# Kernel optimization log

Hardware: AMD Instinct MI355X
Metric: run time of the kernel (lower is better)

Reference implementation:

```python
import jax, jax.numpy as jnp
import numpy as np

# ---- static config (matches init_kwargs) ----
B, H, W = 4, 256, 256
TIN, F, P = 10, 4, 8          # time steps in, forecast steps, patch size
CIN = TIN + 2                  # x concatenated with 2-channel grid
E = 768                        # LATENT_DIMS
NB, BS = 8, 96                 # num_blocks, block_size = E // NB
HP, WP = H // P, W // P
MID = 4 * E                    # channel-mixer hidden (MLP_RATIO=4)
DEPTH = 4
LAM = 0.01                     # softshrink sparsity_threshold


def _gelu(t):
    return jax.nn.gelu(t, approximate=False)  # torch default GELU (erf)


def _shrink(t):
    return jnp.sign(t) * jnp.maximum(jnp.abs(t) - LAM, 0.0)


def _spectral(x, w1, b1, w2, b2):
    """SpectralConvBlockDiag: rfft2 -> block-diag complex MLP (GELU) -> softshrink -> irfft2 + residual."""
    bias = x
    b_, h_, w_, c_ = x.shape
    wf = w_ // 2 + 1
    xf = jnp.fft.rfft2(x, axes=(1, 2), norm='ortho').reshape(b_, h_, wf, NB, BS)
    xr, xi = jnp.real(xf), jnp.imag(xf)
    mm = lambda t, w: jnp.einsum('bhfni,nio->bhfno', t, w)
    # complex linear 1 + GELU on real/imag separately
    o1r = _gelu(mm(xr, w1[0]) - mm(xi, w1[1]) + b1[0])
    o1i = _gelu(mm(xi, w1[0]) + mm(xr, w1[1]) + b1[1])
    # complex linear 2 + softshrink
    o2r = _shrink(mm(o1r, w2[0]) - mm(o1i, w2[1]) + b2[0])
    o2i = _shrink(mm(o1i, w2[0]) + mm(o1r, w2[1]) + b2[1])
    xf = (o2r + 1j * o2i).reshape(b_, h_, wf, c_)
    out = jnp.fft.irfft2(xf, s=(h_, w_), axes=(1, 2), norm='ortho')
    return out + bias


def setup_inputs() -> dict:
    key = jax.random.key(0)
    ks = jax.random.split(key, 20)
    s = 0.02
    f32 = jnp.float32
    return {
        'x': jax.random.normal(ks[0], (B, H, W, TIN), f32),
        'grid': jax.random.uniform(ks[1], (B, H, W, 2), f32),
        'conv_w': s * jax.random.normal(ks[2], (E, CIN, P, P), f32),
        'conv_b': s * jax.random.normal(ks[3], (E,), f32),
        'pos_emb': s * jax.random.normal(ks[4], (HP, WP, E), f32),
        'w1': s * jax.random.normal(ks[5], (DEPTH, 2, NB, BS, BS), f32),
        'b1': s * jax.random.normal(ks[6], (DEPTH, 2, NB, BS), f32),
        'w2': s * jax.random.normal(ks[7], (DEPTH, 2, NB, BS, BS), f32),
        'b2': s * jax.random.normal(ks[8], (DEPTH, 2, NB, BS), f32),
        'fc1_w': s * jax.random.normal(ks[9], (DEPTH, E, MID), f32),
        'fc1_b': s * jax.random.normal(ks[10], (DEPTH, MID), f32),
        'fc2_w': s * jax.random.normal(ks[11], (DEPTH, MID, E), f32),
        'fc2_b': s * jax.random.normal(ks[12], (DEPTH, E), f32),
        'head_w1': s * jax.random.normal(ks[13], (E, 2 * E), f32),
        'head_b1': s * jax.random.normal(ks[14], (2 * E,), f32),
        'head_w2': s * jax.random.normal(ks[15], (2 * E, P * P), f32),
        'head_b2': s * jax.random.normal(ks[16], (P * P,), f32),
    }


def reference(x, grid, conv_w, conv_b, pos_emb, w1, b1, w2, b2,
              fc1_w, fc1_b, fc2_w, fc2_b, head_w1, head_b1, head_w2, head_b2):
    # concat grid channels and patch-embed (conv stride==kernel == patch einsum)
    z = jnp.concatenate([x, grid], axis=-1)                  # (B,H,W,CIN)
    patches = z.reshape(B, HP, P, WP, P, CIN)
    t = jnp.einsum('bhpwqc,ecpq->bhwe', patches, conv_w) + conv_b + pos_emb  # (B,HP,WP,E)
    states = []
    for _ in range(F):
        for d in range(DEPTH):                               # AFNOBoundariesBlock (no residual, identity norms)
            t = _spectral(t, w1[d], b1[d], w2[d], b2[d])
            t = _gelu(t @ fc1_w[d] + fc1_b[d]) @ fc2_w[d] + fc2_b[d]
        states.append(t)
    ls = jnp.stack(states, axis=1)                           # (B,F,HP,WP,E)
    h = _gelu(ls @ head_w1 + head_b1) @ head_w2 + head_b2    # (B,F,HP,WP,P*P)
    h = h.reshape(B, F, HP, WP, P, P, 1)
    h = jnp.transpose(h, (0, 6, 2, 4, 3, 5, 1)).reshape(B, 1, H, W, F)
    return jnp.squeeze(h, axis=1)                            # (B,H,W,F)
```

## Files before the change

### kernel.cpp

```cpp
#include <hip/hip_runtime.h>
#include <hip/hip_bf16.h>
#include <math.h>


typedef __attribute__((ext_vector_type(8))) _Float16 half8;
typedef __attribute__((ext_vector_type(4))) _Float16 half4v;
typedef __attribute__((ext_vector_type(4))) float float4v;

__device__ __forceinline__ float gelu_f(float v) {
    return 0.5f * v * (1.0f + erff(v * 0.70710678118654752f));
}
__device__ __forceinline__ float shrink_f(float v) {
    return (v > 0.01f) ? (v - 0.01f) : ((v < -0.01f) ? (v + 0.01f) : 0.0f);
}

#define STEP32 0.19634954084936207f

__device__ __forceinline__ void async16(const void* g, void* l) {
    __builtin_amdgcn_global_load_lds(
        (const __attribute__((address_space(1))) unsigned int*)g,
        (__attribute__((address_space(3))) unsigned int*)l, 16, 0, 0);
}

__global__ __launch_bounds__(256) void gather_patch(const float* __restrict__ x,
        const float* __restrict__ grd, _Float16* __restrict__ A)
{
    int idx = blockIdx.x * 256 + threadIdx.x;
    int j   = idx % 768;
    int tok = idx / 768;
    int c = j >> 6, p = (j >> 3) & 7, q = j & 7;
    int wp = tok & 31, hp = (tok >> 5) & 31, b = tok >> 10;
    int hh = hp * 8 + p, ww = wp * 8 + q;
    float v;
    if (c < 10) v = x[((b * 256 + hh) * 256 + ww) * 10 + c];
    else        v = grd[((b * 256 + hh) * 256 + ww) * 2 + (c - 10)];
    A[idx] = (_Float16)v;
}

__global__ __launch_bounds__(256) void dft_fwd_w(const _Float16* __restrict__ th,
        _Float16* __restrict__ Xr, _Float16* __restrict__ Xi)
{
    __shared__ float2 lut[32];
    int bh = blockIdx.x;
    int tid = threadIdx.x;
    if (tid < 32) { float a = tid * STEP32; lut[tid] = make_float2(cosf(a), sinf(a)); }
    __syncthreads();
    int b = bh >> 5, h = bh & 31;
    int c = blockIdx.y * 256 + tid;
    float v[32];
    #pragma unroll
    for (int w = 0; w < 32; ++w) v[w] = (float)th[(bh * 32 + w) * 768 + c];
    for (int kw = 0; kw <= 16; ++kw) {
        float ar = 0.f, ai = 0.f;
        #pragma unroll
        for (int w = 0; w < 32; ++w) {
            float2 cs = lut[(kw * w) & 31];
            ar += v[w] * cs.x;
            ai -= v[w] * cs.y;
        }
        size_t g = ((size_t)(b * 17 + kw) * 32 + h) * 768 + c;
        Xr[g] = (_Float16)(ar * 0.03125f);
        Xi[g] = (_Float16)(ai * 0.03125f);
    }
}

__global__ __launch_bounds__(256) void idft_w_mfma(const _Float16* __restrict__ Yr,
        const _Float16* __restrict__ Yi, _Float16* __restrict__ th)
{
    __shared__ alignas(16) _Float16 Yt[192 * 40];
    __shared__ alignas(16) _Float16 El[32 * 40];

    const int tid  = threadIdx.x;
    const int wave = tid >> 6;
    const int lane = tid & 63;
    const int lr   = lane & 15;
    const int quad = lane >> 4;

    const int bh = blockIdx.x;
    const int b  = bh >> 5, h = bh & 31;
    const int c0 = blockIdx.y * 192;

    for (int i = tid; i < 1024; i += 256) {
        int w = i >> 5, s = i & 31;
        float val;
        if (s <= 16) {
            float g = (s == 0 || s == 16) ? 1.f : 2.f;
            val = g * cosf(((w * s) & 31) * STEP32) * 0.03125f;
        } else {
            int k = s - 16;
            val = -2.f * sinf(((w * k) & 31) * STEP32) * 0.03125f;
        }
        El[w * 40 + s] = (_Float16)val;
    }

    #pragma unroll
    for (int i = 0; i < 3; ++i) {
        int u    = tid + i * 256;
        int slot = u / 24;
        int cg   = u % 24;
        const _Float16* src;
        if (slot < 17) src = Yr + ((size_t)(b * 17 + slot) * 32 + h) * 768;
        else           src = Yi + ((size_t)(b * 17 + (slot - 16)) * 32 + h) * 768;
        half8 v = *(const half8*)(src + c0 + cg * 8);
        #pragma unroll
        for (int e = 0; e < 8; ++e) {
            int el = e ^ (cg & 7);
            Yt[(cg * 8 + el) * 40 + slot] = v[el];
        }
    }
    __syncthreads();

    half8 af[2], bf[3];
    #pragma unroll
    for (int m = 0; m < 2; ++m)
        af[m] = *(const half8*)&El[(m * 16 + lr) * 40 + quad * 8];
    #pragma unroll
    for (int n = 0; n < 3; ++n)
        bf[n] = *(const half8*)&Yt[(wave * 48 + n * 16 + lr) * 40 + quad * 8];
    float4v acc[2][3];
    #pragma unroll
    for (int m = 0; m < 2; ++m)
        #pragma unroll
        for (int n = 0; n < 3; ++n) {
            float4v z = {0.f, 0.f, 0.f, 0.f};
            acc[m][n] = __builtin_amdgcn_mfma_f32_16x16x32_f16(af[m], bf[n], z, 0, 0, 0);
        }

    #pragma unroll
    for (int m = 0; m < 2; ++m)
        #pragma unroll
        for (int n = 0; n < 3; ++n) {
            int c = c0 + wave * 48 + n * 16 + lr;
            #pragma unroll
            for (int r = 0; r < 4; ++r) {
                int w = m * 16 + quad * 4 + r;
                size_t gi = (size_t)(bh * 32 + w) * 768 + c;
                th[gi] = (_Float16)(acc[m][n][r] + (float)th[gi]);
            }
        }
}

__global__ __launch_bounds__(256) void prep_specw(const float* __restrict__ w1,
        const float* __restrict__ w2, _Float16* __restrict__ out)
{
    __shared__ float tile[96][97];
    int mid = blockIdx.x;
    int n  = mid & 7;
    int ri = (mid >> 3) & 1;
    int l  = (mid >> 4) & 1;
    int d  = mid >> 5;
    const float* src = (l ? w2 : w1) + ((size_t)(d * 2 + ri) * 8 + n) * 9216;
    for (int idx = threadIdx.x; idx < 9216; idx += 256)
        tile[idx / 96][idx % 96] = src[idx];
    __syncthreads();
    _Float16* dst = out + (size_t)mid * 9216;
    for (int idx = threadIdx.x; idx < 9216; idx += 256)
        dst[idx] = (_Float16)tile[idx % 96][idx / 96];
}

__global__ __launch_bounds__(768) void spec_fused(
        _Float16* __restrict__ Xr, _Float16* __restrict__ Xi,
        const _Float16* __restrict__ W1r, const _Float16* __restrict__ W1i,
        const _Float16* __restrict__ W2r, const _Float16* __restrict__ W2i,
        const float* __restrict__ b1r, const float* __restrict__ b1i,
        const float* __restrict__ b2r, const float* __restrict__ b2i)
{
    __shared__ alignas(16) _Float16 Ec[1024], Es[1024];
    __shared__ alignas(16) _Float16 XTr[3840], XTi[3840];
    __shared__ alignas(16) _Float16 Zr[3328], Zi[3328];
    __shared__ alignas(16) _Float16 Sr[3328], Si[3328];

    const int bk = blockIdx.x;
    const int n  = blockIdx.y;
    const int tid = threadIdx.x;
    const int wave = tid >> 6, lane = tid & 63;
    const int wr = wave / 6;
    const int wo = wave % 6;
    const int lr = lane & 15, quad = lane >> 4;
    const size_t base = (size_t)bk * 24576 + n * 96;

    for (int i = tid; i < 1024; i += 768) {
        int kh = i >> 5, h = i & 31;
        float a = ((kh * h) & 31) * STEP32;
        Ec[i] = (_Float16)cosf(a);
        Es[i] = (_Float16)sinf(a);
    }
    for (int i = tid; i < 384; i += 768) {
        int h = i / 12, cc = (i % 12) * 8;
        half8 vr = *(const half8*)(Xr + base + (size_t)h * 768 + cc);
        half8 vi = *(const half8*)(Xi + base + (size_t)h * 768 + cc);
        #pragma unroll
        for (int e = 0; e < 8; ++e) {
            XTr[(cc + e) * 40 + h] = vr[e];
            XTi[(cc + e) * 40 + h] = vi[e];
        }
    }
    __syncthreads();

    const _Float16* w1r = W1r + (size_t)n * 9216;
    const _Float16* w1i = W1i + (size_t)n * 9216;
    const _Float16* w2r = W2r + (size_t)n * 9216;
    const _Float16* w2i = W2i + (size_t)n * 9216;

    half8 eC = *(const half8*)&Ec[(wr * 16 + lr) * 32 + quad * 8];
    half8 eS = *(const half8*)&Es[(wr * 16 + lr) * 32 + quad * 8];
    half8 eSn = -eS;

    {
        int c = wo * 16 + lr;
        float4v zr = {0,0,0,0}, zi = {0,0,0,0};
        half8 xr = *(const half8*)&XTr[c * 40 + quad * 8];
        half8 xi = *(const half8*)&XTi[c * 40 + quad * 8];
        zr = __builtin_amdgcn_mfma_f32_16x16x32_f16(eC,  xr, zr, 0, 0, 0);
        zr = __builtin_amdgcn_mfma_f32_16x16x32_f16(eS,  xi, zr, 0, 0, 0);
        zi = __builtin_amdgcn_mfma_f32_16x16x32_f16(eC,  xi, zi, 0, 0, 0);
        zi = __builtin_amdgcn_mfma_f32_16x16x32_f16(eSn, xr, zi, 0, 0, 0);
        #pragma unroll
        for (int r = 0; r < 4; ++r) {
            int kh = wr * 16 + quad * 4 + r;
            Zr[kh * 104 + c] = (_Float16)zr[r];
            Zi[kh * 104 + c] = (_Float16)zi[r];
        }
    }
    __syncthreads();

    {
        int o = wo * 16 + lr;
        float4v sr = {0,0,0,0}, si = {0,0,0,0};
        #pragma unroll
        for (int kc = 0; kc < 3; ++kc) {
            half8 ar = *(const half8*)&Zr[(wr * 16 + lr) * 104 + kc * 32 + quad * 8];
            half8 ai = *(const half8*)&Zi[(wr * 16 + lr) * 104 + kc * 32 + quad * 8];
            half8 ain = -ai;
            half8 br = *(const half8*)&w1r[o * 96 + kc * 32 + quad * 8];
            half8 bi = *(const half8*)&w1i[o * 96 + kc * 32 + quad * 8];
            sr = __builtin_amdgcn_mfma_f32_16x16x32_f16(ar,  br, sr, 0, 0, 0);
            sr = __builtin_amdgcn_mfma_f32_16x16x32_f16(ain, bi, sr, 0, 0, 0);
            si = __builtin_amdgcn_mfma_f32_16x16x32_f16(ai,  br, si, 0, 0, 0);
            si = __builtin_amdgcn_mfma_f32_16x16x32_f16(ar,  bi, si, 0, 0, 0);
        }
        float br = b1r[n * 96 + o], bi = b1i[n * 96 + o];
        #pragma unroll
        for (int r = 0; r < 4; ++r) {
            int kh = wr * 16 + quad * 4 + r;
            Sr[kh * 104 + o] = (_Float16)gelu_f(sr[r] + br);
            Si[kh * 104 + o] = (_Float16)gelu_f(si[r] + bi);
        }
    }
    __syncthreads();

    {
        int o = wo * 16 + lr;
        float4v tr = {0,0,0,0}, ti = {0,0,0,0};
        #pragma unroll
        for (int kc = 0; kc < 3; ++kc) {
            half8 ar = *(const half8*)&Sr[(wr * 16 + lr) * 104 + kc * 32 + quad * 8];
            half8 ai = *(const half8*)&Si[(wr * 16 + lr) * 104 + kc * 32 + quad * 8];
            half8 ain = -ai;
            half8 br = *(const half8*)&w2r[o * 96 + kc * 32 + quad * 8];
            half8 bi = *(const half8*)&w2i[o * 96 + kc * 32 + quad * 8];
            tr = __builtin_amdgcn_mfma_f32_16x16x32_f16(ar,  br, tr, 0, 0, 0);
            tr = __builtin_amdgcn_mfma_f32_16x16x32_f16(ain, bi, tr, 0, 0, 0);
            ti = __builtin_amdgcn_mfma_f32_16x16x32_f16(ai,  br, ti, 0, 0, 0);
            ti = __builtin_amdgcn_mfma_f32_16x16x32_f16(ar,  bi, ti, 0, 0, 0);
        }
        float br = b2r[n * 96 + o], bi = b2i[n * 96 + o];
        #pragma unroll
        for (int r = 0; r < 4; ++r) {
            int kh = wr * 16 + quad * 4 + r;
            XTr[o * 40 + kh] = (_Float16)shrink_f(tr[r] + br);
            XTi[o * 40 + kh] = (_Float16)shrink_f(ti[r] + bi);
        }
    }
    __syncthreads();

    {
        int c = wo * 16 + lr;
        float4v yr = {0,0,0,0}, yi = {0,0,0,0};
        half8 t2r = *(const half8*)&XTr[c * 40 + quad * 8];
        half8 t2i = *(const half8*)&XTi[c * 40 + quad * 8];
        yr = __builtin_amdgcn_mfma_f32_16x16x32_f16(eC,  t2r, yr, 0, 0, 0);
        yr = __builtin_amdgcn_mfma_f32_16x16x32_f16(eSn, t2i, yr, 0, 0, 0);
        yi = __builtin_amdgcn_mfma_f32_16x16x32_f16(eC,  t2i, yi, 0, 0, 0);
        yi = __builtin_amdgcn_mfma_f32_16x16x32_f16(eS,  t2r, yi, 0, 0, 0);
        #pragma unroll
        for (int r = 0; r < 4; ++r) {
            int h = wr * 16 + quad * 4 + r;
            Zr[h * 104 + c] = (_Float16)yr[r];
            Zi[h * 104 + c] = (_Float16)yi[r];
        }
    }
    __syncthreads();

    for (int i = tid; i < 384; i += 768) {
        int h = i / 12, cc = (i % 12) * 8;
        half8 vr = *(const half8*)&Zr[h * 104 + cc];
        half8 vi = *(const half8*)&Zi[h * 104 + cc];
        *(half8*)(Xr + base + (size_t)h * 768 + cc) = vr;
        *(half8*)(Xi + base + (size_t)h * 768 + cc) = vi;
    }
}

__global__ __launch_bounds__(256) void cvt_f16(const float* __restrict__ in,
        _Float16* __restrict__ out)
{
    int i = blockIdx.x * 256 + threadIdx.x;
    float4 v = ((const float4*)in)[i];
    half4v o;
    o.x = (_Float16)v.x; o.y = (_Float16)v.y; o.z = (_Float16)v.z; o.w = (_Float16)v.w;
    ((half4v*)out)[i] = o;
}

__global__ __launch_bounds__(256) void cvt_transpose(const float* __restrict__ in,
        _Float16* __restrict__ out, int K, int N)
{
    __shared__ float tile[32][33];
    int kb = blockIdx.x * 32, nb = blockIdx.y * 32;
    int tx = threadIdx.x & 31, ty = threadIdx.x >> 5;
    #pragma unroll
    for (int r = 0; r < 32; r += 8)
        tile[ty + r][tx] = in[(size_t)(kb + ty + r) * N + nb + tx];
    __syncthreads();
    #pragma unroll
    for (int r = 0; r < 32; r += 8)
        out[(size_t)(nb + ty + r) * K + kb + tx] = (_Float16)tile[tx][ty + r];
}

__global__ __launch_bounds__(256) void cvt_transpose8(const float* __restrict__ fc1w,
        const float* __restrict__ fc2w, _Float16* __restrict__ WtAll)
{
    __shared__ float tile[32][33];
    const int z  = blockIdx.y;
    const int l  = z & 1;
    const int d  = z >> 1;
    const int K  = l ? 3072 : 768;
    const int N  = l ? 768 : 3072;
    const float* src = (l ? fc2w : fc1w) + (size_t)d * 2359296;
    _Float16*    dst = WtAll + (size_t)z * 2359296;
    const int nt = N >> 5;
    int kb = (blockIdx.x / nt) * 32;
    int nb = (blockIdx.x % nt) * 32;
    int tx = threadIdx.x & 31, ty = threadIdx.x >> 5;
    #pragma unroll
    for (int r = 0; r < 32; r += 8)
        tile[ty + r][tx] = src[(size_t)(kb + ty + r) * N + nb + tx];
    __syncthreads();
    #pragma unroll
    for (int r = 0; r < 32; r += 8)
        dst[(size_t)(nb + ty + r) * K + kb + tx] = (_Float16)tile[tx][ty + r];
}

template<int BN, int ACT, int POS>
__global__ __launch_bounds__(512, 4) void gemm128d(const _Float16* __restrict__ A,
        const _Float16* __restrict__ Bt, const float* __restrict__ bias,
        const float* __restrict__ pos, _Float16* __restrict__ C16,
        int M, int N, int K)
{
    constexpr int WN  = BN / 4;
    constexpr int FN  = WN / 16;
    constexpr int AU  = 2;
    constexpr int BU  = BN / 64;
    constexpr int LPT = AU + BU;
    __shared__ _Float16 Al[2][128 * 64];
    __shared__ _Float16 Bl[2][BN * 64];

    const int tid  = threadIdx.x;
    const int wave = tid >> 6;
    const int lane = tid & 63;
    const int wr   = wave >> 2;
    const int wc   = wave & 3;
    const int lr   = lane & 15;
    const int quad = lane >> 4;

    const int gx = gridDim.x, gy = gridDim.y, nbk = gx * gy;
    int bx = blockIdx.x, by = blockIdx.y;
    if (!(gy & 3) && !(gx & 1)) {
        int id = by * gx + bx;
        int xcd = id & 7, j = id >> 3;
        int cols = gx >> 1;
        int rows = gy >> 2;
        int jr = j / cols, jc = j % cols;
        by = (xcd >> 1) * rows + jr;
        bx = (xcd & 1) * cols + jc;
    } else if (!(nbk & 7)) {
        int id  = by * gx + bx;
        int id2 = (id & 7) * (nbk >> 3) + (id >> 3);
        by = id2 / gx; bx = id2 % gx;
    }
    const int row0 = by * 128;
    const int col0 = bx * BN;

    const int srow = lane >> 3;
    const int schk = (lane & 7) ^ (srow & 7);
    const _Float16* Ab = A  + (size_t)(row0 + wave * 8 + srow) * K + schk * 8;
    const _Float16* Bb = Bt + (size_t)(col0 + wave * 8 + srow) * K + schk * 8;

    auto stage = [&](int b, int kt) {
        const int k0 = kt * 64;
        #pragma unroll
        for (int u = 0; u < AU; ++u)
            async16(Ab + (size_t)u * 64 * K + k0, &Al[b][(u * 64 + wave * 8) * 64]);
        #pragma unroll
        for (int u = 0; u < BU; ++u)
            async16(Bb + (size_t)u * 64 * K + k0, &Bl[b][(u * 64 + wave * 8) * 64]);
    };

    float4v acc[4][FN];
    #pragma unroll
    for (int m = 0; m < 4; ++m)
        #pragma unroll
        for (int n = 0; n < FN; ++n) {
            float4v z = {0.f, 0.f, 0.f, 0.f};
            acc[m][n] = z;
        }

    auto compute = [&](int cb) {
        #pragma unroll
        for (int ks = 0; ks < 2; ++ks) {
            const int cA = ((ks * 4 + quad) ^ (lr & 7)) * 8;
            half8 bf[FN];
            #pragma unroll
            for (int n = 0; n < FN; ++n)
                bf[n] = *(const half8*)&Bl[cb][(wc * WN + n * 16 + lr) * 64 + cA];
            half8 af[4];
            #pragma unroll
            for (int m = 0; m < 4; ++m)
                af[m] = *(const half8*)&Al[cb][(wr * 64 + m * 16 + lr) * 64 + cA];
            __builtin_amdgcn_s_setprio(1);
            #pragma unroll
            for (int m = 0; m < 4; ++m)
                #pragma unroll
                for (int n = 0; n < FN; ++n)
                    acc[m][n] = __builtin_amdgcn_mfma_f32_16x16x32_f16(af[m], bf[n], acc[m][n], 0, 0, 0);
            __builtin_amdgcn_s_setprio(0);
        }
    };

    const int NT = K >> 6;
    stage(0, 0);
    stage(1, 1);
    for (int t = 0; t < NT; ++t) {
        if (t + 1 < NT) {
            if constexpr (LPT == 5) asm volatile("s_waitcnt vmcnt(5)" ::: "memory");
            else                    asm volatile("s_waitcnt vmcnt(3)" ::: "memory");
        } else {
            asm volatile("s_waitcnt vmcnt(0)" ::: "memory");
        }
        __builtin_amdgcn_s_barrier();
        compute(t & 1);
        __builtin_amdgcn_s_barrier();
        if (t + 2 < NT) stage(t & 1, t + 2);
    }

    #pragma unroll
    for (int n = 0; n < FN; ++n) {
        int col = col0 + wc * WN + n * 16 + lr;
        float bj = bias[col];
        #pragma unroll
        for (int m = 0; m < 4; ++m) {
            int row = row0 + wr * 64 + m * 16 + quad * 4;
            #pragma unroll
            for (int r = 0; r < 4; ++r) {
                float v = acc[m][n][r] + bj;
                if (POS) v += pos[(size_t)((row + r) & 1023) * N + col];
                if (ACT) v = gelu_f(v);
                C16[(size_t)(row + r) * N + col] = (_Float16)v;
            }
        }
    }
}

__global__ __launch_bounds__(256, 3) void fc2_fused(const _Float16* __restrict__ A,
        const _Float16* __restrict__ Bt, const float* __restrict__ bias,
        _Float16* __restrict__ C16, _Float16* __restrict__ XR,
        _Float16* __restrict__ XI)
{
    constexpr int K = 3072;
    constexpr int NT = 48;
    __shared__ _Float16 Al[2][64 * 64];
    __shared__ _Float16 Bl[2][64 * 64];
    __shared__ alignas(16) _Float16 Tl[2 * 64 * 40];
    __shared__ alignas(16) _Float16 ECl[1024], ESl[1024];

    const int tid  = threadIdx.x;
    const int wave = tid >> 6;
    const int lane = tid & 63;
    const int wr   = wave >> 1;
    const int wc   = wave & 1;
    const int lr   = lane & 15;
    const int quad = lane >> 4;

    for (int i = tid; i < 1024; i += 256) {
        int kw = i >> 5, w = i & 31;
        float a = ((kw * w) & 31) * STEP32;
        ECl[i] = (_Float16)(cosf(a) * 0.03125f);
        ESl[i] = (_Float16)(-sinf(a) * 0.03125f);
    }

    const int gx = gridDim.x, gy = gridDim.y;
    int bx = blockIdx.x, by = blockIdx.y;
    {
        int id = by * gx + bx;
        int xcd = id & 7, j = id >> 3;
        int cols = gx >> 1;
        int rows = gy >> 2;
        int jr = j / cols, jc = j % cols;
        by = (xcd >> 1) * rows + jr;
        bx = (xcd & 1) * cols + jc;
    }
    const int row0 = by * 64;
    const int col0 = bx * 64;

    const int srow = lane >> 3;
    const int schk = (lane & 7) ^ srow;
    const _Float16* Ab = A  + (size_t)(row0 + wave * 8 + srow) * K + schk * 8;
    const _Float16* Bb = Bt + (size_t)(col0 + wave * 8 + srow) * K + schk * 8;

    auto stage = [&](int b, int kt) {
        const int k0 = kt * 64;
        #pragma unroll
        for (int u = 0; u < 2; ++u)
            async16(Ab + (size_t)u * 32 * K + k0, &Al[b][(u * 32 + wave * 8) * 64]);
        #pragma unroll
        for (int u = 0; u < 2; ++u)
            async16(Bb + (size_t)u * 32 * K + k0, &Bl[b][(u * 32 + wave * 8) * 64]);
    };

    float4v acc[2][2];
    #pragma unroll
    for (int m = 0; m < 2; ++m)
        #pragma unroll
        for (int n = 0; n < 2; ++n) {
            float4v z = {0.f, 0.f, 0.f, 0.f};
            acc[m][n] = z;
        }

    auto compute = [&](int cb) {
        #pragma unroll
        for (int ks = 0; ks < 2; ++ks) {
            const int cA = ((ks * 4 + quad) ^ (lr & 7)) * 8;
            half8 bf[2], af[2];
            #pragma unroll
            for (int n = 0; n < 2; ++n)
                bf[n] = *(const half8*)&Bl[cb][(wc * 32 + n * 16 + lr) * 64 + cA];
            #pragma unroll
            for (int m = 0; m < 2; ++m)
                af[m] = *(const half8*)&Al[cb][(wr * 32 + m * 16 + lr) * 64 + cA];
            __builtin_amdgcn_s_setprio(1);
            #pragma unroll
            for (int m = 0; m < 2; ++m)
                #pragma unroll
                for (int n = 0; n < 2; ++n)
                    acc[m][n] = __builtin_amdgcn_mfma_f32_16x16x32_f16(af[m], bf[n], acc[m][n], 0, 0, 0);
            __builtin_amdgcn_s_setprio(0);
        }
    };

    stage(0, 0);
    stage(1, 1);
    for (int t = 0; t < NT; ++t) {
        if (t + 1 < NT) asm volatile("s_waitcnt vmcnt(4)" ::: "memory");
        else            asm volatile("s_waitcnt vmcnt(0)" ::: "memory");
        __builtin_amdgcn_s_barrier();
        compute(t & 1);
        __builtin_amdgcn_s_barrier();
        if (t + 2 < NT) stage(t & 1, t + 2);
    }

    #pragma unroll
    for (int n = 0; n < 2; ++n) {
        int cc  = wc * 32 + n * 16 + lr;
        int col = col0 + cc;
        float bj = bias[col];
        #pragma unroll
        for (int m = 0; m < 2; ++m) {
            int row = row0 + wr * 32 + m * 16 + quad * 4;
            #pragma unroll
            for (int r = 0; r < 4; ++r) {
                float v = acc[m][n][r] + bj;
                C16[(size_t)(row + r) * 768 + col] = (_Float16)v;
                int lrow = row + r - row0;
                Tl[((lrow >> 5) * 64 + cc) * 40 + (lrow & 31)] = (_Float16)v;
            }
        }
    }
    __syncthreads();

    const int h     = wave >> 1;
    const int cbase = (wave & 1) * 32;
    const int b     = row0 >> 10;
    const int hp    = ((row0 >> 5) & 31) + h;
    half8 eC0 = *(const half8*)&ECl[lr * 32 + quad * 8];
    half8 eC1 = *(const half8*)&ECl[(16 + lr) * 32 + quad * 8];
    half8 eS0 = *(const half8*)&ESl[lr * 32 + quad * 8];
    half8 eS1 = *(const half8*)&ESl[(16 + lr) * 32 + quad * 8];
    float4v xr[2][2], xi[2][2];
    #pragma unroll
    for (int m = 0; m < 2; ++m)
        #pragma unroll
        for (int nj = 0; nj < 2; ++nj) {
            float4v z = {0.f, 0.f, 0.f, 0.f};
            xr[m][nj] = z; xi[m][nj] = z;
        }
    #pragma unroll
    for (int nj = 0; nj < 2; ++nj) {
        half8 tb = *(const half8*)&Tl[(h * 64 + cbase + nj * 16 + lr) * 40 + quad * 8];
        xr[0][nj] = __builtin_amdgcn_mfma_f32_16x16x32_f16(eC0, tb, xr[0][nj], 0, 0, 0);
        xr[1][nj] = __builtin_amdgcn_mfma_f32_16x16x32_f16(eC1, tb, xr[1][nj], 0, 0, 0);
        xi[0][nj] = __builtin_amdgcn_mfma_f32_16x16x32_f16(eS0, tb, xi[0][nj], 0, 0, 0);
        xi[1][nj] = __builtin_amdgcn_mfma_f32_16x16x32_f16(eS1, tb, xi[1][nj], 0, 0, 0);
    }
    #pragma unroll
    for (int m = 0; m < 2; ++m)
        #pragma unroll
        for (int r = 0; r < 4; ++r) {
            int kw = m * 16 + quad * 4 + r;
            if (kw < 17) {
                #pragma unroll
                for (int nj = 0; nj < 2; ++nj) {
                    int c = col0 + cbase + nj * 16 + lr;
                    size_t g = ((size_t)(b * 17 + kw) * 32 + hp) * 768 + c;
                    XR[g] = (_Float16)xr[m][nj][r];
                    XI[g] = (_Float16)xi[m][nj][r];
                }
            }
        }
}

__global__ __launch_bounds__(256, 4) void head2_k(const _Float16* __restrict__ A,
        const _Float16* __restrict__ Bt, const float* __restrict__ bias,
        float* __restrict__ C32, int f_idx)
{
    constexpr int K = 1536;
    constexpr int NT = 24;
    __shared__ _Float16 Al[2][64 * 64];
    __shared__ _Float16 Bl[2][64 * 64];

    const int tid  = threadIdx.x;
    const int wave = tid >> 6;
    const int lane = tid & 63;
    const int wr   = wave >> 1;
    const int wc   = wave & 1;
    const int lr   = lane & 15;
    const int quad = lane >> 4;

    const int row0 = blockIdx.x * 64;

    const int srow = lane >> 3;
    const int schk = (lane & 7) ^ srow;
    const _Float16* Ab = A  + (size_t)(row0 + wave * 8 + srow) * K + schk * 8;
    const _Float16* Bb = Bt + (size_t)(wave * 8 + srow) * K + schk * 8;

    auto stage = [&](int b, int kt) {
        const int k0 = kt * 64;
        #pragma unroll
        for (int u = 0; u < 2; ++u)
            async16(Ab + (size_t)u * 32 * K + k0, &Al[b][(u * 32 + wave * 8) * 64]);
        #pragma unroll
        for (int u = 0; u < 2; ++u)
            async16(Bb + (size_t)u * 32 * K + k0, &Bl[b][(u * 32 + wave * 8) * 64]);
    };

    float4v acc[2][2];
    #pragma unroll
    for (int m = 0; m < 2; ++m)
        #pragma unroll
        for (int n = 0; n < 2; ++n) {
            float4v z = {0.f, 0.f, 0.f, 0.f};
            acc[m][n] = z;
        }

    auto compute = [&](int cb) {
        #pragma unroll
        for (int ks = 0; ks < 2; ++ks) {
            const int cA = ((ks * 4 + quad) ^ (lr & 7)) * 8;
            half8 bf[2], af[2];
            #pragma unroll
            for (int n = 0; n < 2; ++n)
                bf[n] = *(const half8*)&Bl[cb][(wc * 32 + n * 16 + lr) * 64 + cA];
            #pragma unroll
            for (int m = 0; m < 2; ++m)
                af[m] = *(const half8*)&Al[cb][(wr * 32 + m * 16 + lr) * 64 + cA];
            #pragma unroll
            for (int m = 0; m < 2; ++m)
                #pragma unroll
                for (int n = 0; n < 2; ++n)
                    acc[m][n] = __builtin_amdgcn_mfma_f32_16x16x32_f16(af[m], bf[n], acc[m][n], 0, 0, 0);
        }
    };

    stage(0, 0);
    stage(1, 1);
    for (int t = 0; t < NT; ++t) {
        if (t + 1 < NT) asm volatile("s_waitcnt vmcnt(4)" ::: "memory");
        else            asm volatile("s_waitcnt vmcnt(0)" ::: "memory");
        __builtin_amdgcn_s_barrier();
        compute(t & 1);
        __builtin_amdgcn_s_barrier();
        if (t + 2 < NT) stage(t & 1, t + 2);
    }

    #pragma unroll
    for (int n = 0; n < 2; ++n) {
        int col = wc * 32 + n * 16 + lr;
        float bj = bias[col];
        int p = col >> 3, q = col & 7;
        #pragma unroll
        for (int m = 0; m < 2; ++m) {
            int row = row0 + wr * 32 + m * 16 + quad * 4;
            #pragma unroll
            for (int r = 0; r < 4; ++r) {
                float v = acc[m][n][r] + bj;
                int rowv = row + r;
                int bq = rowv >> 10, hp = (rowv >> 5) & 31, wp = rowv & 31;
                C32[(((size_t)(bq * 256 + hp * 8 + p)) * 256 + wp * 8 + q) * 4 + f_idx] = v;
            }
        }
    }
}

template<int BN, int OUT_MODE, int ACT>
__global__ __launch_bounds__(256) void gemm_h(const _Float16* __restrict__ A,
        const _Float16* __restrict__ Bt, const float* __restrict__ bias,
        const float* __restrict__ pos, float* __restrict__ C32,
        _Float16* __restrict__ C16, _Float16* __restrict__ XR,
        _Float16* __restrict__ XI, int M, int N, int K, int f_idx)
{
    constexpr int WN  = BN / 2;
    constexpr int FN  = WN / 16;
    constexpr int NBJ = BN / 64;
    constexpr int LPT = 2 + NBJ;
    __shared__ _Float16 Al[4][128 * 32];
    __shared__ _Float16 Bl[4][BN * 32];

    const int tid  = threadIdx.x;
    const int wave = tid >> 6;
    const int lane = tid & 63;
    const int wr   = wave >> 1;
    const int wc   = wave & 1;
    const int lr   = lane & 15;
    const int quad = lane >> 4;

    const int gx = gridDim.x, gy = gridDim.y, nbk = gx * gy;
    int bx = blockIdx.x, by = blockIdx.y;
    if (!(gy & 3) && !(gx & 1)) {
        int id = by * gx + bx;
        int xcd = id & 7, j = id >> 3;
        int cols = gx >> 1;
        int rows = gy >> 2;
        int jr = j / cols, jc = j % cols;
        by = (xcd >> 1) * rows + jr;
        bx = (xcd & 1) * cols + jc;
    } else if (!(nbk & 7)) {
        int id  = by * gx + bx;
        int id2 = (id & 7) * (nbk >> 3) + (id >> 3);
        by = id2 / gx; bx = id2 % gx;
    }
    const int row0 = by * 128;
    const int col0 = bx * BN;

    const int srow = lane >> 2;
    const int skof = ((lane & 3) ^ (srow & 3)) * 8;

    auto stage = [&](int b, int kt) {
        const int k0 = kt << 5;
        #pragma unroll
        for (int j = 0; j < 2; ++j)
            async16(A + (size_t)(row0 + j * 64 + wave * 16 + srow) * K + k0 + skof,
                    &Al[b][(j * 64 + wave * 16) * 32]);
        #pragma unroll
        for (int j = 0; j < NBJ; ++j)
            async16(Bt + (size_t)(col0 + j * 64 + wave * 16 + srow) * K + k0 + skof,
                    &Bl[b][(j * 64 + wave * 16) * 32]);
    };

    float4v acc[4][FN];
    #pragma unroll
    for (int i = 0; i < 4; ++i)
        #pragma unroll
        for (int j = 0; j < FN; ++j) {
            float4v z = {0.f, 0.f, 0.f, 0.f};
            acc[i][j] = z;
        }

    auto compute = [&](int cb) {
        const int cA = (quad ^ (lr & 3)) * 8;
        half8 af[4], bf[FN];
        #pragma unroll
        for (int i = 0; i < 4; ++i)
            af[i] = *(const half8*)&Al[cb][(wr * 64 + i * 16 + lr) * 32 + cA];
        #pragma unroll
        for (int j = 0; j < FN; ++j)
            bf[j] = *(const half8*)&Bl[cb][(wc * WN + j * 16 + lr) * 32 + cA];
        #pragma unroll
        for (int i = 0; i < 4; ++i)
            #pragma unroll
            for (int j = 0; j < FN; ++j)
                acc[i][j] = __builtin_amdgcn_mfma_f32_16x16x32_f16(af[i], bf[j], acc[i][j], 0, 0, 0);
    };

    const int KT = K >> 5;
    stage(0, 0); stage(1, 1); stage(2, 2);
    int kt = 0;
    for (; kt < KT - 3; ++kt) {
        stage((kt + 3) & 3, kt + 3);
        if constexpr (LPT == 4) asm volatile("s_waitcnt vmcnt(12)" ::: "memory");
        else                    asm volatile("s_waitcnt vmcnt(9)"  ::: "memory");
        __builtin_amdgcn_s_barrier();
        compute(kt & 3);
        asm volatile("" ::: "memory");
        __builtin_amdgcn_s_barrier();
    }
    if constexpr (LPT == 4) asm volatile("s_waitcnt vmcnt(8)" ::: "memory");
    else                    asm volatile("s_waitcnt vmcnt(6)" ::: "memory");
    __builtin_amdgcn_s_barrier();
    compute(kt & 3); ++kt;
    asm volatile("" ::: "memory");
    __builtin_amdgcn_s_barrier();
    if constexpr (LPT == 4) asm volatile("s_waitcnt vmcnt(4)" ::: "memory");
    else                    asm volatile("s_waitcnt vmcnt(3)" ::: "memory");
    __builtin_amdgcn_s_barrier();
    compute(kt & 3); ++kt;
    asm volatile("" ::: "memory");
    __builtin_amdgcn_s_barrier();
    asm volatile("s_waitcnt vmcnt(0)" ::: "memory");
    __builtin_amdgcn_s_barrier();
    compute(kt & 3);

    #pragma unroll
    for (int j = 0; j < FN; ++j) {
        int col = col0 + wc * WN + j * 16 + lr;
        float bj = bias[col];
        #pragma unroll
        for (int i = 0; i < 4; ++i) {
            int row = row0 + wr * 64 + i * 16 + quad * 4;
            #pragma unroll
            for (int r = 0; r < 4; ++r) {
                float v = acc[i][j][r] + bj;
                if (pos) v += pos[(size_t)((row + r) & 1023) * N + col];
                if (ACT) v = gelu_f(v);
                if (OUT_MODE == 3) {
                    int rowv = row + r;
                    int bq = rowv >> 10, hp = (rowv >> 5) & 31, wp = rowv & 31;
                    int p = col >> 3, q = col & 7;
                    C32[(((size_t)(bq * 256 + hp * 8 + p)) * 256 + wp * 8 + q) * 4 + f_idx] = v;
                } else {
                    C16[(size_t)(row + r) * N + col] = (_Float16)v;
                }
            }
        }
    }
}

extern "C" void kernel_launch(void* const* d_in, const int* in_sizes, int n_in,
                              void* d_out, int out_size, void* d_ws, size_t ws_size,
                              hipStream_t stream) {
    const float* x        = (const float*)d_in[0];
    const float* grd      = (const float*)d_in[1];
    const float* conv_w   = (const float*)d_in[2];
    const float* conv_b   = (const float*)d_in[3];
    const float* pos_emb  = (const float*)d_in[4];
    const float* w1       = (const float*)d_in[5];
    const float* b1       = (const float*)d_in[6];
    const float* w2       = (const float*)d_in[7];
    const float* b2       = (const float*)d_in[8];
    const float* fc1_w    = (const float*)d_in[9];
    const float* fc1_b    = (const float*)d_in[10];
    const float* fc2_w    = (const float*)d_in[11];
    const float* fc2_b    = (const float*)d_in[12];
    const float* head_w1  = (const float*)d_in[13];
    const float* head_b1  = (const float*)d_in[14];
    const float* head_w2  = (const float*)d_in[15];
    const float* head_b2  = (const float*)d_in[16];
    float* out = (float*)d_out;
    float* ws  = (float*)d_ws;

    float* pf = ws;
    _Float16* t_h     = (_Float16*)pf; pf += 1572864;
    _Float16* Wsp     = (_Float16*)pf; pf += 589824;
    _Float16* h1t     = (_Float16*)pf; pf += 589824;
    _Float16* h2t     = (_Float16*)pf; pf += 49152;
    _Float16* convw_h = (_Float16*)pf; pf += 294912;
    float* alias    = pf;              pf += 6291456;
    _Float16* hid_h = (_Float16*)alias;
    _Float16* WtAll = (_Float16*)pf;   pf += 9437184;
    _Float16* xa_r_fb = (_Float16*)alias;
    _Float16* xa_i_fb = (_Float16*)(alias + 835584);
    _Float16* xa_r_fu = (_Float16*)pf;
    _Float16* xa_i_fu = (_Float16*)(pf + 835584);
    size_t full_total = (size_t)(pf - ws) + 1671168;
    bool full = ws_size >= full_total * 4ull;
    _Float16* xa_r = full ? xa_r_fu : xa_r_fb;
    _Float16* xa_i = full ? xa_i_fu : xa_i_fb;
    _Float16* A_h  = (_Float16*)alias;

    prep_specw<<<dim3(128), 256, 0, stream>>>(w1, w2, Wsp);
    cvt_f16<<<dim3(576), 256, 0, stream>>>(conv_w, convw_h);
    cvt_transpose<<<dim3(24, 48), 256, 0, stream>>>(head_w1, h1t, 768, 1536);
    cvt_transpose<<<dim3(48, 2), 256, 0, stream>>>(head_w2, h2t, 1536, 64);
    cvt_transpose8<<<dim3(2304, 8), 256, 0, stream>>>(fc1_w, fc2_w, WtAll);
    gather_patch<<<dim3(12288), 256, 0, stream>>>(x, grd, A_h);
    gemm128d<64, 0, 1><<<dim3(12, 32), 512, 0, stream>>>(
        A_h, convw_h, conv_b, pos_emb, t_h, 4096, 768, 768);
    dft_fwd_w<<<dim3(128, 3), 256, 0, stream>>>(t_h, xa_r, xa_i);

    for (int f = 0; f < 4; ++f) {
        for (int d = 0; d < 4; ++d) {
            spec_fused<<<dim3(68, 8), 768, 0, stream>>>(
                xa_r, xa_i,
                Wsp + (size_t)(d * 4 + 0) * 73728, Wsp + (size_t)(d * 4 + 1) * 73728,
                Wsp + (size_t)(d * 4 + 2) * 73728, Wsp + (size_t)(d * 4 + 3) * 73728,
                b1 + d * 1536, b1 + d * 1536 + 768,
                b2 + d * 1536, b2 + d * 1536 + 768);
            idft_w_mfma<<<dim3(128, 4), 256, 0, stream>>>(xa_r, xa_i, t_h);
            gemm128d<192, 1, 0><<<dim3(16, 32), 512, 0, stream>>>(
                t_h, WtAll + (size_t)(2 * d) * 2359296, fc1_b + d * 3072,
                nullptr, hid_h, 4096, 3072, 768);
            if (full) {
                fc2_fused<<<dim3(12, 64), 256, 0, stream>>>(
                    hid_h, WtAll + (size_t)(2 * d + 1) * 2359296, fc2_b + d * 768,
                    t_h, xa_r, xa_i);
            } else {
                gemm_h<64, 1, 0><<<dim3(12, 32), 256, 0, stream>>>(
                    hid_h, WtAll + (size_t)(2 * d + 1) * 2359296, fc2_b + d * 768,
                    nullptr, nullptr, t_h, nullptr, nullptr, 4096, 768, 3072, 0);
                dft_fwd_w<<<dim3(128, 3), 256, 0, stream>>>(t_h, xa_r, xa_i);
            }
        }
        gemm128d<64, 1, 0><<<dim3(24, 32), 512, 0, stream>>>(
            t_h, h1t, head_b1, nullptr, hid_h, 4096, 1536, 768);
        head2_k<<<dim3(64), 256, 0, stream>>>(
            hid_h, h2t, head_b2, out, f);
    }
}
```

Baseline: 1.693 ms.

## Add triple-buffered fc1 GEMM kernel with XCD-aware tile remapping

Replaces the generic double-buffered fc1 GEMM with a specialized kernel that uses three LDS stages with async global-to-LDS loads issued two tiles ahead, split across the two k-substeps. Block indices are remapped so each XCD gets a contiguous region of output tiles, aimed at better L2 reuse. It also raises MFMA priority around the compute loop. The larger LDS footprint (about 120KB) limits occupancy to one block per CU, which is the tradeoff against deeper prefetch.

```diff
diff --git a/kernel.cpp b/kernel.cpp
--- a/kernel.cpp
+++ b/kernel.cpp
@@ -348,6 +348,114 @@
     #pragma unroll
     for (int r = 0; r < 32; r += 8)
         dst[(size_t)(nb + ty + r) * K + kb + tx] = (_Float16)tile[tx][ty + r];
+}
+
+__global__ __launch_bounds__(512, 1) void fc1_deep(const _Float16* __restrict__ A,
+        const _Float16* __restrict__ Bt, const float* __restrict__ bias,
+        _Float16* __restrict__ C16)
+{
+    constexpr int K = 768, NT = 12, N = 3072;
+    __shared__ _Float16 Al[3][128 * 64];
+    __shared__ _Float16 Bl[3][192 * 64];
+
+    const int tid  = threadIdx.x;
+    const int wave = tid >> 6;
+    const int lane = tid & 63;
+    const int wr   = wave >> 2;
+    const int wc   = wave & 3;
+    const int lr   = lane & 15;
+    const int quad = lane >> 4;
+
+    const int gx = gridDim.x, gy = gridDim.y;
+    int bx = blockIdx.x, by = blockIdx.y;
+    {
+        int id = by * gx + bx;
+        int xcd = id & 7, j = id >> 3;
+        int cols = gx >> 1;
+        int rows = gy >> 2;
+        int jr = j / cols, jc = j % cols;
+        by = (xcd >> 1) * rows + jr;
+        bx = (xcd & 1) * cols + jc;
+    }
+    const int row0 = by * 128;
+    const int col0 = bx * 192;
+
+    const int srow = lane >> 3;
+    const int schk = (lane & 7) ^ (srow & 7);
+    const _Float16* Ab = A  + (size_t)(row0 + wave * 8 + srow) * K + schk * 8;
+    const _Float16* Bb = Bt + (size_t)(col0 + wave * 8 + srow) * K + schk * 8;
+
+    auto stageA3 = [&](int b, int kt) {
+        const int k0 = kt * 64;
+        async16(Ab + k0,                       &Al[b][(wave * 8) * 64]);
+        async16(Ab + (size_t)64 * K + k0,      &Al[b][(64 + wave * 8) * 64]);
+        async16(Bb + k0,                       &Bl[b][(wave * 8) * 64]);
+    };
+    auto stageB2 = [&](int b, int kt) {
+        const int k0 = kt * 64;
+        async16(Bb + (size_t)64 * K + k0,      &Bl[b][(64 + wave * 8) * 64]);
+        async16(Bb + (size_t)128 * K + k0,     &Bl[b][(128 + wave * 8) * 64]);
+    };
+
+    float4v acc[4][3];
+    #pragma unroll
+    for (int m = 0; m < 4; ++m)
+        #pragma unroll
+        for (int n = 0; n < 3; ++n) {
+            float4v z = {0.f, 0.f, 0.f, 0.f};
+            acc[m][n] = z;
+        }
+
+    stageA3(0, 0); stageB2(0, 0);
+    stageA3(1, 1); stageB2(1, 1);
+
+    int cur = 0;
+    for (int t = 0; t < NT; ++t) {
+        if (t + 1 < NT) asm volatile("s_waitcnt vmcnt(5)" ::: "memory");
+        else            asm volatile("s_waitcnt vmcnt(0)" ::: "memory");
+        __builtin_amdgcn_s_barrier();
+        int nxt = cur + 2; if (nxt >= 3) nxt -= 3;
+        #pragma unroll
+        for (int ks = 0; ks < 2; ++ks) {
+            const int cA = ((ks * 4 + quad) ^ (lr & 7)) * 8;
+            half8 bf[3];
+            #pragma unroll
+            for (int n = 0; n < 3; ++n)
+                bf[n] = *(const half8*)&Bl[cur][(wc * 48 + n * 16 + lr) * 64 + cA];
+            half8 af[4];
+            #pragma unroll
+            for (int m = 0; m < 4; ++m)
+                af[m] = *(const half8*)&Al[cur][(wr * 64 + m * 16 + lr) * 64 + cA];
+            if (t + 2 < NT) {
+                if (ks == 0) stageA3(nxt, t + 2);
+                else         stageB2(nxt, t + 2);
+            }
+            __builtin_amdgcn_s_setprio(1);
+            #pragma unroll
+            for (int m = 0; m < 4; ++m)
+                #pragma unroll
+                for (int n = 0; n < 3; ++n)
+                    acc[m][n] = __builtin_amdgcn_mfma_f32_16x16x32_f16(af[m], bf[n], acc[m][n], 0, 0, 0);
+            __builtin_amdgcn_s_setprio(0);
+        }
+        ++cur; if (cur >= 3) cur -= 3;
+    }
+
+    #pragma unroll
+    for (int n = 0; n < 3; ++n) {
+        int col = col0 + wc * 48 + n * 16 + lr;
+        float bj = bias[col];
+        #pragma unroll
+        for (int m = 0; m < 4; ++m) {
+            int row = row0 + wr * 64 + m * 16 + quad * 4;
+            #pragma unroll
+            for (int r = 0; r < 4; ++r) {
+                float v = acc[m][n][r] + bj;
+                v = gelu_f(v);
+                C16[(size_t)(row + r) * N + col] = (_Float16)v;
+            }
+        }
+    }
 }
 
 template<int BN, int ACT, int POS>
@@ -913,9 +1021,8 @@
                 b1 + d * 1536, b1 + d * 1536 + 768,
                 b2 + d * 1536, b2 + d * 1536 + 768);
             idft_w_mfma<<<dim3(128, 4), 256, 0, stream>>>(xa_r, xa_i, t_h);
-            gemm128d<192, 1, 0><<<dim3(16, 32), 512, 0, stream>>>(
-                t_h, WtAll + (size_t)(2 * d) * 2359296, fc1_b + d * 3072,
-                nullptr, hid_h, 4096, 3072, 768);
+            fc1_deep<<<dim3(16, 32), 512, 0, stream>>>(
+                t_h, WtAll + (size_t)(2 * d) * 2359296, fc1_b + d * 3072, hid_h);
             if (full) {
                 fc2_fused<<<dim3(12, 64), 256, 0, stream>>>(
                     hid_h, WtAll + (size_t)(2 * d + 1) * 2359296, fc2_b + d * 768,
```

Result: no change. 1.723 ms (+1.7%).
